# Kernel tuning notes

Measured on AMD Instinct MI355X. Metric: run time of the kernel, lower is better.

Reference implementation:

```python
import jax, jax.numpy as jnp
import numpy as np

B, M, D, P, T = 512, 16, 128, 16, 4096
GAMMA = 1.0  # similarity_size


def setup_inputs() -> dict:
    key = jax.random.key(0)
    k1, k2, k3, k4, k5 = jax.random.split(key, 5)
    phi = jax.random.normal(k1, (B, P), dtype=jnp.float32)
    state = jax.random.normal(k2, (B, D), dtype=jnp.float32)
    trajectories = jax.random.normal(k3, (T, D), dtype=jnp.float32)
    # Stand-in per-model KAARMA state-transition parameters (linear recurrent + input map, tanh)
    A = jax.random.normal(k4, (M, D, D), dtype=jnp.float32) * (1.0 / np.sqrt(D))
    B_in = jax.random.normal(k5, (M, P, D), dtype=jnp.float32) * (1.0 / np.sqrt(P))
    return {"phi": phi, "state": state, "trajectories": trajectories, "A": A, "B_in": B_in}


def reference(phi, state, trajectories, A, B_in):
    # per-model state update: new_state[b,m,:] = tanh(state @ A_m + phi @ B_m)
    new_state = jnp.tanh(
        jnp.einsum("bd,mdh->bmh", state, A) + jnp.einsum("bp,mph->bmh", phi, B_in)
    )  # [B, M, D]
    # RBF similarity vs trajectory set via ||s||^2 + ||t||^2 - 2 s.t (single batched GEMM)
    s_sq = jnp.sum(new_state * new_state, axis=-1, keepdims=True)      # [B, M, 1]
    t_sq = jnp.sum(trajectories * trajectories, axis=-1)               # [T]
    cross = jnp.einsum("bmd,td->bmt", new_state, trajectories)         # [B, M, T]
    sq_dist = jnp.maximum(s_sq + t_sq[None, None, :] - 2.0 * cross, 0.0)
    sim = jnp.exp(-GAMMA * sq_dist)                                    # [B, M, T]
    output = sim.reshape(phi.shape[0], -1)                             # [B, M*T]
    return output, new_state
```

## Files before the change

kernel.cpp:

```cpp
#include <hip/hip_runtime.h>
#include <hip/hip_bf16.h>
#include <cstdint>
#include <cstddef>

#define NB 512
#define NM 16
#define ND 128
#define NP 16
#define NT 4096

typedef __bf16 bf16x8 __attribute__((ext_vector_type(8)));
typedef float f32x4 __attribute__((ext_vector_type(4)));

static_assert(sizeof(bf16x8) == 16, "bf16x8 must be 16B");

__device__ __forceinline__ void gload_lds16(const void* g, void* l) {
  __builtin_amdgcn_global_load_lds(
      (const __attribute__((address_space(1))) unsigned int*)g,
      (__attribute__((address_space(3))) unsigned int*)l, 16, 0, 0);
}

__global__ __launch_bounds__(256) void prep_kernel(
    const float* __restrict__ phi, const float* __restrict__ state,
    const float* __restrict__ traj, const float* __restrict__ A,
    const float* __restrict__ Bin, float* __restrict__ ns_out,
    __bf16* __restrict__ ns_bf, __bf16* __restrict__ tj_bf,
    float* __restrict__ s_sq, float* __restrict__ t_sq) {
  __shared__ alignas(16) float sSt[16 * 128];
  __shared__ alignas(16) float sPhi[16 * 16];
  __shared__ alignas(16) float sRes[16 * 128];
  const int tid = threadIdx.x;
  const int bx = blockIdx.x;

  if (bx < 512) {
    const int m = bx & 15;
    const int b0 = (bx >> 4) * 16;
    const float4* S4 = (const float4*)(state + (size_t)b0 * 128);
    float4* sSt4 = (float4*)sSt;
    sSt4[tid] = S4[tid];
    sSt4[tid + 256] = S4[tid + 256];
    sPhi[tid] = phi[b0 * 16 + tid];
    __syncthreads();

    const int h2 = tid & 63;
    const int rgrp = tid >> 6;
    const float* Ap = A + (size_t)m * 16384 + h2;
    const float* Bp = Bin + (size_t)m * 2048 + h2;

    float acc[2][4];
#pragma unroll
    for (int hi = 0; hi < 2; ++hi)
#pragma unroll
      for (int j = 0; j < 4; ++j) acc[hi][j] = 0.f;

#pragma unroll 4
    for (int c = 0; c < 32; ++c) {
      float a0[4], a1[4];
#pragma unroll
      for (int u = 0; u < 4; ++u) {
        a0[u] = Ap[(size_t)(c * 4 + u) * 128];
        a1[u] = Ap[(size_t)(c * 4 + u) * 128 + 64];
      }
#pragma unroll
      for (int j = 0; j < 4; ++j) {
        const f32x4 sv = *(const f32x4*)&sSt[(rgrp * 4 + j) * 128 + c * 4];
#pragma unroll
        for (int u = 0; u < 4; ++u) {
          acc[0][j] = fmaf(sv[u], a0[u], acc[0][j]);
          acc[1][j] = fmaf(sv[u], a1[u], acc[1][j]);
        }
      }
    }
#pragma unroll
    for (int pc = 0; pc < 4; ++pc) {
      float b0v[4], b1v[4];
#pragma unroll
      for (int u = 0; u < 4; ++u) {
        b0v[u] = Bp[(size_t)(pc * 4 + u) * 128];
        b1v[u] = Bp[(size_t)(pc * 4 + u) * 128 + 64];
      }
#pragma unroll
      for (int j = 0; j < 4; ++j) {
        const f32x4 pv = *(const f32x4*)&sPhi[(rgrp * 4 + j) * 16 + pc * 4];
#pragma unroll
        for (int u = 0; u < 4; ++u) {
          acc[0][j] = fmaf(pv[u], b0v[u], acc[0][j]);
          acc[1][j] = fmaf(pv[u], b1v[u], acc[1][j]);
        }
      }
    }

#pragma unroll
    for (int j = 0; j < 4; ++j) {
      const int row = rgrp * 4 + j;
      const int R = (b0 + row) * 16 + m;
      const float v0 = tanhf(acc[0][j]);
      const float v1 = tanhf(acc[1][j]);
      ns_out[(size_t)R * 128 + h2] = v0;
      ns_out[(size_t)R * 128 + h2 + 64] = v1;
      sRes[row * 128 + h2] = v0;
      sRes[row * 128 + h2 + 64] = v1;
      float s = v0 * v0 + v1 * v1;
#pragma unroll
      for (int o = 32; o > 0; o >>= 1) s += __shfl_xor(s, o);
      if (h2 == 0) s_sq[R] = s;
    }
    __syncthreads();

    {
      const int row = tid >> 4;
      const int kb = tid & 15;
      const f32x4 r0 = *(const f32x4*)&sRes[row * 128 + kb * 8];
      const f32x4 r1 = *(const f32x4*)&sRes[row * 128 + kb * 8 + 4];
      bf16x8 o;
#pragma unroll
      for (int i = 0; i < 4; ++i) {
        o[i] = (__bf16)r0[i];
        o[i + 4] = (__bf16)r1[i];
      }
      const int R = (b0 + row) * 16 + m;
      *(bf16x8*)(ns_bf + (size_t)R * 128 + ((kb ^ m) * 8)) = o;
    }
  } else {
    const int t0 = (bx - 512) * 128;
    const int t = t0 + (tid >> 1);
    const int half = tid & 1;
    float s = 0.f;
#pragma unroll
    for (int q = 0; q < 8; ++q) {
      const int kb = half * 8 + q;
      const f32x4 v0 = *(const f32x4*)&traj[(size_t)t * 128 + kb * 8];
      const f32x4 v1 = *(const f32x4*)&traj[(size_t)t * 128 + kb * 8 + 4];
      s += v0[0] * v0[0] + v0[1] * v0[1] + v0[2] * v0[2] + v0[3] * v0[3];
      s += v1[0] * v1[0] + v1[1] * v1[1] + v1[2] * v1[2] + v1[3] * v1[3];
      bf16x8 o;
#pragma unroll
      for (int i = 0; i < 4; ++i) {
        o[i] = (__bf16)v0[i];
        o[i + 4] = (__bf16)v1[i];
      }
      *(bf16x8*)(tj_bf + (size_t)t * 128 + ((kb ^ (t & 15)) * 8)) = o;
    }
    s += __shfl_xor(s, 1);
    if (half == 0) t_sq[t] = s;
  }
}

__global__ __launch_bounds__(256, 1) void sim_kernel(
    const __bf16* __restrict__ ns_bf, const __bf16* __restrict__ tj_bf,
    const float* __restrict__ s_sq, const float* __restrict__ t_sq,
    float* __restrict__ out) {
  __shared__ alignas(16) __bf16 sNS[128 * 128];
  __shared__ alignas(16) __bf16 sT[2][128 * 128];
  const int tid = threadIdx.x;
  const int lane = tid & 63;
  const int w = tid >> 6;
  const int p = blockIdx.x;
  const int R0 = (p >> 2) * 128;
  const int Cg = (p & 3) * 8;
  const int rbase = (w >> 1) * 64;
  const int cbase = (w & 1) * 64;
  const int l15 = lane & 15;
  const int quad = lane >> 4;

  const char* gNS = (const char*)(ns_bf + (size_t)R0 * 128);
  const char* gT0 = (const char*)(tj_bf + (size_t)(Cg * 128) * 128);
#pragma unroll
  for (int it = 0; it < 8; ++it) {
    const int off = it * 4096 + w * 1024;
    gload_lds16(gNS + off + lane * 16, (char*)sNS + off);
    gload_lds16(gT0 + off + lane * 16, (char*)sT[0] + off);
  }
  __syncthreads();

  bf16x8 af[4][4];
#pragma unroll
  for (int ks = 0; ks < 4; ++ks)
#pragma unroll
    for (int i = 0; i < 4; ++i)
      af[ks][i] = *(const bf16x8*)&sNS[(rbase + i * 16 + l15) * 128 +
                                       (((quad + ks * 4) ^ l15) * 8)];
  float sqr[4];
#pragma unroll
  for (int ri = 0; ri < 4; ++ri)
    sqr[ri] = s_sq[R0 + rbase + ri * 16 + l15];

#pragma unroll
  for (int t = 0; t < 8; ++t) {
    const int cur = t & 1;
    if (t + 1 < 8) {
      const char* gT = (const char*)(tj_bf + (size_t)((Cg + t + 1) * 128) * 128);
#pragma unroll
      for (int it = 0; it < 8; ++it) {
        const int off = it * 4096 + w * 1024;
        gload_lds16(gT + off + lane * 16, (char*)sT[cur ^ 1] + off);
      }
    }

    f32x4 acc[4][4];
#pragma unroll
    for (int i = 0; i < 4; ++i)
#pragma unroll
      for (int j = 0; j < 4; ++j) acc[i][j] = (f32x4){0.f, 0.f, 0.f, 0.f};

    const __bf16* sB = sT[cur];
#pragma unroll
    for (int ks = 0; ks < 4; ++ks) {
      bf16x8 bfr[4];
#pragma unroll
      for (int i = 0; i < 4; ++i)
        bfr[i] = *(const bf16x8*)&sB[(cbase + i * 16 + l15) * 128 +
                                     (((quad + ks * 4) ^ l15) * 8)];
#pragma unroll
      for (int ri = 0; ri < 4; ++ri)
#pragma unroll
        for (int ci = 0; ci < 4; ++ci)
          acc[ri][ci] = __builtin_amdgcn_mfma_f32_16x16x32_bf16(
              bfr[ci], af[ks][ri], acc[ri][ci], 0, 0, 0);
    }

    const int C0 = (Cg + t) * 128;
    f32x4 tq[4];
#pragma unroll
    for (int ci = 0; ci < 4; ++ci)
      tq[ci] = *(const f32x4*)&t_sq[C0 + cbase + ci * 16 + quad * 4];
#pragma unroll
    for (int ri = 0; ri < 4; ++ri) {
      const float sq = sqr[ri];
      float* orow = out + (size_t)(R0 + rbase + ri * 16 + l15) * NT + C0;
#pragma unroll
      for (int ci = 0; ci < 4; ++ci) {
        const int t4 = cbase + ci * 16 + quad * 4;
        f32x4 r;
#pragma unroll
        for (int k = 0; k < 4; ++k) {
          const float d = fmaxf(sq + tq[ci][k] - 2.f * acc[ri][ci][k], 0.f);
          r[k] = __expf(-d);
        }
        *(f32x4*)&orow[t4] = r;
      }
    }
    __syncthreads();
  }
}

extern "C" void kernel_launch(void* const* d_in, const int* in_sizes, int n_in,
                              void* d_out, int out_size, void* d_ws,
                              size_t ws_size, hipStream_t stream) {
  (void)in_sizes; (void)n_in; (void)out_size; (void)ws_size;
  const float* phi   = (const float*)d_in[0];
  const float* state = (const float*)d_in[1];
  const float* traj  = (const float*)d_in[2];
  const float* A     = (const float*)d_in[3];
  const float* Bin   = (const float*)d_in[4];

  float* out = (float*)d_out;
  float* out_ns = out + (size_t)NB * NM * NT;

  char* ws = (char*)d_ws;
  __bf16* ns_bf = (__bf16*)ws;
  __bf16* tj_bf = (__bf16*)(ws + (2u << 20));
  float* s_sq   = (float*)(ws + (3u << 20));
  float* t_sq   = (float*)(ws + (3u << 20) + (32u << 10));

  prep_kernel<<<544, 256, 0, stream>>>(phi, state, traj, A, Bin, out_ns, ns_bf,
                                       tj_bf, s_sq, t_sq);
  sim_kernel<<<256, 256, 0, stream>>>(ns_bf, tj_bf, s_sq, t_sq, out);
}
```

Baseline: 175.0 us.

## Fuse state-update GEMV into similarity kernel and split trajectory prep out

The state update (tanh of state@A + phi@B) now runs inside the similarity kernel. Each block computes 32 rows of new_state for one model and keeps them in LDS as swizzled bf16, so the bf16 state buffer and s_sq no longer round-trip through global memory. Trajectory conversion moves to its own small kernel. The sim tile shrinks to 32 rows by 2048 columns with 512 blocks at two blocks per CU. The cost is that each block pair recomputes the same state GEMV, and the A/B reads are redundant across the two column halves.

Measured after the change: 175.4 us. No clear change (+0.2%).

```diff
diff --git a/kernel.cpp b/kernel.cpp
--- a/kernel.cpp
+++ b/kernel.cpp
@@ -20,224 +20,205 @@
       (__attribute__((address_space(3))) unsigned int*)l, 16, 0, 0);
 }
 
-__global__ __launch_bounds__(256) void prep_kernel(
+__global__ __launch_bounds__(256) void traj_kernel(
+    const float* __restrict__ traj, __bf16* __restrict__ tj_bf,
+    float* __restrict__ t_sq) {
+  const int tid = threadIdx.x;
+  const int t = blockIdx.x * 128 + (tid >> 1);
+  const int half = tid & 1;
+  float s = 0.f;
+#pragma unroll
+  for (int q = 0; q < 8; ++q) {
+    const int kb = half * 8 + q;
+    const f32x4 v0 = *(const f32x4*)&traj[(size_t)t * 128 + kb * 8];
+    const f32x4 v1 = *(const f32x4*)&traj[(size_t)t * 128 + kb * 8 + 4];
+    s += v0[0] * v0[0] + v0[1] * v0[1] + v0[2] * v0[2] + v0[3] * v0[3];
+    s += v1[0] * v1[0] + v1[1] * v1[1] + v1[2] * v1[2] + v1[3] * v1[3];
+    bf16x8 o;
+#pragma unroll
+    for (int i = 0; i < 4; ++i) {
+      o[i] = (__bf16)v0[i];
+      o[i + 4] = (__bf16)v1[i];
+    }
+    *(bf16x8*)(tj_bf + (size_t)t * 128 + ((kb ^ (t & 15)) * 8)) = o;
+  }
+  s += __shfl_xor(s, 1);
+  if (half == 0) t_sq[t] = s;
+}
+
+__global__ __launch_bounds__(256, 2) void fused_kernel(
     const float* __restrict__ phi, const float* __restrict__ state,
-    const float* __restrict__ traj, const float* __restrict__ A,
-    const float* __restrict__ Bin, float* __restrict__ ns_out,
-    __bf16* __restrict__ ns_bf, __bf16* __restrict__ tj_bf,
-    float* __restrict__ s_sq, float* __restrict__ t_sq) {
-  __shared__ alignas(16) float sSt[16 * 128];
-  __shared__ alignas(16) float sPhi[16 * 16];
-  __shared__ alignas(16) float sRes[16 * 128];
-  const int tid = threadIdx.x;
-  const int bx = blockIdx.x;
-
-  if (bx < 512) {
-    const int m = bx & 15;
-    const int b0 = (bx >> 4) * 16;
-    const float4* S4 = (const float4*)(state + (size_t)b0 * 128);
-    float4* sSt4 = (float4*)sSt;
-    sSt4[tid] = S4[tid];
-    sSt4[tid + 256] = S4[tid + 256];
-    sPhi[tid] = phi[b0 * 16 + tid];
-    __syncthreads();
-
-    const int h2 = tid & 63;
-    const int rgrp = tid >> 6;
-    const float* Ap = A + (size_t)m * 16384 + h2;
-    const float* Bp = Bin + (size_t)m * 2048 + h2;
-
-    float acc[2][4];
-#pragma unroll
-    for (int hi = 0; hi < 2; ++hi)
-#pragma unroll
-      for (int j = 0; j < 4; ++j) acc[hi][j] = 0.f;
-
-#pragma unroll 4
-    for (int c = 0; c < 32; ++c) {
-      float a0[4], a1[4];
-#pragma unroll
-      for (int u = 0; u < 4; ++u) {
-        a0[u] = Ap[(size_t)(c * 4 + u) * 128];
-        a1[u] = Ap[(size_t)(c * 4 + u) * 128 + 64];
-      }
-#pragma unroll
-      for (int j = 0; j < 4; ++j) {
-        const f32x4 sv = *(const f32x4*)&sSt[(rgrp * 4 + j) * 128 + c * 4];
-#pragma unroll
-        for (int u = 0; u < 4; ++u) {
-          acc[0][j] = fmaf(sv[u], a0[u], acc[0][j]);
-          acc[1][j] = fmaf(sv[u], a1[u], acc[1][j]);
-        }
-      }
-    }
-#pragma unroll
-    for (int pc = 0; pc < 4; ++pc) {
-      float b0v[4], b1v[4];
-#pragma unroll
-      for (int u = 0; u < 4; ++u) {
-        b0v[u] = Bp[(size_t)(pc * 4 + u) * 128];
-        b1v[u] = Bp[(size_t)(pc * 4 + u) * 128 + 64];
-      }
-#pragma unroll
-      for (int j = 0; j < 4; ++j) {
-        const f32x4 pv = *(const f32x4*)&sPhi[(rgrp * 4 + j) * 16 + pc * 4];
-#pragma unroll
-        for (int u = 0; u < 4; ++u) {
-          acc[0][j] = fmaf(pv[u], b0v[u], acc[0][j]);
-          acc[1][j] = fmaf(pv[u], b1v[u], acc[1][j]);
-        }
-      }
-    }
-
-#pragma unroll
-    for (int j = 0; j < 4; ++j) {
-      const int row = rgrp * 4 + j;
-      const int R = (b0 + row) * 16 + m;
-      const float v0 = tanhf(acc[0][j]);
-      const float v1 = tanhf(acc[1][j]);
-      ns_out[(size_t)R * 128 + h2] = v0;
-      ns_out[(size_t)R * 128 + h2 + 64] = v1;
-      sRes[row * 128 + h2] = v0;
-      sRes[row * 128 + h2 + 64] = v1;
-      float s = v0 * v0 + v1 * v1;
-#pragma unroll
-      for (int o = 32; o > 0; o >>= 1) s += __shfl_xor(s, o);
-      if (h2 == 0) s_sq[R] = s;
-    }
-    __syncthreads();
-
-    {
-      const int row = tid >> 4;
-      const int kb = tid & 15;
-      const f32x4 r0 = *(const f32x4*)&sRes[row * 128 + kb * 8];
-      const f32x4 r1 = *(const f32x4*)&sRes[row * 128 + kb * 8 + 4];
-      bf16x8 o;
-#pragma unroll
-      for (int i = 0; i < 4; ++i) {
-        o[i] = (__bf16)r0[i];
-        o[i + 4] = (__bf16)r1[i];
-      }
-      const int R = (b0 + row) * 16 + m;
-      *(bf16x8*)(ns_bf + (size_t)R * 128 + ((kb ^ m) * 8)) = o;
-    }
-  } else {
-    const int t0 = (bx - 512) * 128;
-    const int t = t0 + (tid >> 1);
-    const int half = tid & 1;
-    float s = 0.f;
-#pragma unroll
-    for (int q = 0; q < 8; ++q) {
-      const int kb = half * 8 + q;
-      const f32x4 v0 = *(const f32x4*)&traj[(size_t)t * 128 + kb * 8];
-      const f32x4 v1 = *(const f32x4*)&traj[(size_t)t * 128 + kb * 8 + 4];
-      s += v0[0] * v0[0] + v0[1] * v0[1] + v0[2] * v0[2] + v0[3] * v0[3];
-      s += v1[0] * v1[0] + v1[1] * v1[1] + v1[2] * v1[2] + v1[3] * v1[3];
-      bf16x8 o;
-#pragma unroll
-      for (int i = 0; i < 4; ++i) {
-        o[i] = (__bf16)v0[i];
-        o[i + 4] = (__bf16)v1[i];
-      }
-      *(bf16x8*)(tj_bf + (size_t)t * 128 + ((kb ^ (t & 15)) * 8)) = o;
-    }
-    s += __shfl_xor(s, 1);
-    if (half == 0) t_sq[t] = s;
-  }
-}
-
-__global__ __launch_bounds__(256, 1) void sim_kernel(
-    const __bf16* __restrict__ ns_bf, const __bf16* __restrict__ tj_bf,
-    const float* __restrict__ s_sq, const float* __restrict__ t_sq,
-    float* __restrict__ out) {
-  __shared__ alignas(16) __bf16 sNS[128 * 128];
-  __shared__ alignas(16) __bf16 sT[2][128 * 128];
+    const float* __restrict__ A, const float* __restrict__ Bin,
+    const __bf16* __restrict__ tj_bf, const float* __restrict__ t_sq,
+    float* __restrict__ ns_out, float* __restrict__ out) {
+  __shared__ alignas(16) char smem[75904];
+  char* sT0 = smem;
+  char* sT1 = smem + 32768;
+  float* sSt = (float*)(smem + 32768);
+  __bf16* sNS = (__bf16*)(smem + 65536);
+  float* sSq = (float*)(smem + 73728);
+  float* sPhi = (float*)(smem + 73856);
+
   const int tid = threadIdx.x;
   const int lane = tid & 63;
   const int w = tid >> 6;
   const int p = blockIdx.x;
-  const int R0 = (p >> 2) * 128;
-  const int Cg = (p & 3) * 8;
-  const int rbase = (w >> 1) * 64;
-  const int cbase = (w & 1) * 64;
+  const int pan = p >> 1;
+  const int ch = p & 1;
+  const int m = pan & 15;
+  const int b0 = (pan >> 4) * 32;
+  const int tt0 = ch * 16;
+
+  {
+    const float4* S4 = (const float4*)(state + (size_t)b0 * 128);
+    float4* sSt4 = (float4*)sSt;
+#pragma unroll
+    for (int q = 0; q < 4; ++q) sSt4[tid + q * 256] = S4[tid + q * 256];
+    sPhi[tid] = phi[b0 * 16 + tid];
+    sPhi[tid + 256] = phi[b0 * 16 + tid + 256];
+  }
+  __syncthreads();
+
+  {
+    const char* gT = (const char*)tj_bf + (size_t)tt0 * 32768;
+#pragma unroll
+    for (int it = 0; it < 8; ++it) {
+      const int off = it * 4096 + w * 1024;
+      gload_lds16(gT + off + lane * 16, sT0 + off);
+    }
+  }
+
+  const int h2 = lane;
+  const float* Ap = A + (size_t)m * 16384 + h2;
+  const float* Bp = Bin + (size_t)m * 2048 + h2;
+  float acc0[8], acc1[8];
+#pragma unroll
+  for (int j = 0; j < 8; ++j) { acc0[j] = 0.f; acc1[j] = 0.f; }
+
+#pragma unroll 4
+  for (int c = 0; c < 32; ++c) {
+    float a0[4], a1[4];
+#pragma unroll
+    for (int u = 0; u < 4; ++u) {
+      a0[u] = Ap[(size_t)(c * 4 + u) * 128];
+      a1[u] = Ap[(size_t)(c * 4 + u) * 128 + 64];
+    }
+#pragma unroll
+    for (int j = 0; j < 8; ++j) {
+      const f32x4 sv = *(const f32x4*)&sSt[(w * 8 + j) * 128 + c * 4];
+#pragma unroll
+      for (int u = 0; u < 4; ++u) {
+        acc0[j] = fmaf(sv[u], a0[u], acc0[j]);
+        acc1[j] = fmaf(sv[u], a1[u], acc1[j]);
+      }
+    }
+  }
+#pragma unroll
+  for (int pc = 0; pc < 4; ++pc) {
+    float b0v[4], b1v[4];
+#pragma unroll
+    for (int u = 0; u < 4; ++u) {
+      b0v[u] = Bp[(size_t)(pc * 4 + u) * 128];
+      b1v[u] = Bp[(size_t)(pc * 4 + u) * 128 + 64];
+    }
+#pragma unroll
+    for (int j = 0; j < 8; ++j) {
+      const f32x4 pv = *(const f32x4*)&sPhi[(w * 8 + j) * 16 + pc * 4];
+#pragma unroll
+      for (int u = 0; u < 4; ++u) {
+        acc0[j] = fmaf(pv[u], b0v[u], acc0[j]);
+        acc1[j] = fmaf(pv[u], b1v[u], acc1[j]);
+      }
+    }
+  }
+
+#pragma unroll
+  for (int j = 0; j < 8; ++j) {
+    const int r = w * 8 + j;
+    const int R = (b0 + r) * 16 + m;
+    const float v0 = tanhf(acc0[j]);
+    const float v1 = tanhf(acc1[j]);
+    if (ch == 0) {
+      ns_out[(size_t)R * 128 + h2] = v0;
+      ns_out[(size_t)R * 128 + h2 + 64] = v1;
+    }
+    const int kb0 = h2 >> 3;
+    sNS[r * 128 + ((kb0 ^ (r & 15)) << 3) + (h2 & 7)] = (__bf16)v0;
+    sNS[r * 128 + (((kb0 + 8) ^ (r & 15)) << 3) + (h2 & 7)] = (__bf16)v1;
+    float s = v0 * v0 + v1 * v1;
+#pragma unroll
+    for (int o = 32; o > 0; o >>= 1) s += __shfl_xor(s, o);
+    if (lane == 0) sSq[r] = s;
+  }
+  __syncthreads();
+
   const int l15 = lane & 15;
   const int quad = lane >> 4;
-
-  const char* gNS = (const char*)(ns_bf + (size_t)R0 * 128);
-  const char* gT0 = (const char*)(tj_bf + (size_t)(Cg * 128) * 128);
-#pragma unroll
-  for (int it = 0; it < 8; ++it) {
-    const int off = it * 4096 + w * 1024;
-    gload_lds16(gNS + off + lane * 16, (char*)sNS + off);
-    gload_lds16(gT0 + off + lane * 16, (char*)sT[0] + off);
-  }
-  __syncthreads();
-
-  bf16x8 af[4][4];
+  bf16x8 af[4][2];
 #pragma unroll
   for (int ks = 0; ks < 4; ++ks)
 #pragma unroll
-    for (int i = 0; i < 4; ++i)
-      af[ks][i] = *(const bf16x8*)&sNS[(rbase + i * 16 + l15) * 128 +
-                                       (((quad + ks * 4) ^ l15) * 8)];
-  float sqr[4];
-#pragma unroll
-  for (int ri = 0; ri < 4; ++ri)
-    sqr[ri] = s_sq[R0 + rbase + ri * 16 + l15];
-
-#pragma unroll
-  for (int t = 0; t < 8; ++t) {
-    const int cur = t & 1;
-    if (t + 1 < 8) {
-      const char* gT = (const char*)(tj_bf + (size_t)((Cg + t + 1) * 128) * 128);
+    for (int ri = 0; ri < 2; ++ri)
+      af[ks][ri] = *(const bf16x8*)&sNS[(ri * 16 + l15) * 128 +
+                                        (((quad + ks * 4) ^ l15) * 8)];
+  float sqr[2];
+#pragma unroll
+  for (int ri = 0; ri < 2; ++ri) sqr[ri] = sSq[ri * 16 + l15];
+
+#pragma unroll 2
+  for (int t = 0; t < 16; ++t) {
+    const char* curbuf = (t & 1) ? sT1 : sT0;
+    if (t + 1 < 16) {
+      char* nxt = (t & 1) ? sT0 : sT1;
+      const char* gT = (const char*)tj_bf + (size_t)(tt0 + t + 1) * 32768;
 #pragma unroll
       for (int it = 0; it < 8; ++it) {
         const int off = it * 4096 + w * 1024;
-        gload_lds16(gT + off + lane * 16, (char*)sT[cur ^ 1] + off);
-      }
-    }
-
-    f32x4 acc[4][4];
-#pragma unroll
-    for (int i = 0; i < 4; ++i)
-#pragma unroll
-      for (int j = 0; j < 4; ++j) acc[i][j] = (f32x4){0.f, 0.f, 0.f, 0.f};
-
-    const __bf16* sB = sT[cur];
+        gload_lds16(gT + off + lane * 16, nxt + off);
+      }
+    }
+
+    const __bf16* sB = (const __bf16*)curbuf;
+    f32x4 acc[2][2];
+#pragma unroll
+    for (int i = 0; i < 2; ++i)
+#pragma unroll
+      for (int j = 0; j < 2; ++j) acc[i][j] = (f32x4){0.f, 0.f, 0.f, 0.f};
+
 #pragma unroll
     for (int ks = 0; ks < 4; ++ks) {
-      bf16x8 bfr[4];
-#pragma unroll
-      for (int i = 0; i < 4; ++i)
-        bfr[i] = *(const bf16x8*)&sB[(cbase + i * 16 + l15) * 128 +
-                                     (((quad + ks * 4) ^ l15) * 8)];
-#pragma unroll
-      for (int ri = 0; ri < 4; ++ri)
-#pragma unroll
-        for (int ci = 0; ci < 4; ++ci)
+      bf16x8 bfr[2];
+#pragma unroll
+      for (int ci = 0; ci < 2; ++ci)
+        bfr[ci] = *(const bf16x8*)&sB[(w * 32 + ci * 16 + l15) * 128 +
+                                      (((quad + ks * 4) ^ l15) * 8)];
+#pragma unroll
+      for (int ri = 0; ri < 2; ++ri)
+#pragma unroll
+        for (int ci = 0; ci < 2; ++ci)
           acc[ri][ci] = __builtin_amdgcn_mfma_f32_16x16x32_bf16(
               bfr[ci], af[ks][ri], acc[ri][ci], 0, 0, 0);
     }
 
-    const int C0 = (Cg + t) * 128;
-    f32x4 tq[4];
-#pragma unroll
-    for (int ci = 0; ci < 4; ++ci)
-      tq[ci] = *(const f32x4*)&t_sq[C0 + cbase + ci * 16 + quad * 4];
-#pragma unroll
-    for (int ri = 0; ri < 4; ++ri) {
+    const int C0 = (tt0 + t) * 128;
+    f32x4 tq[2];
+#pragma unroll
+    for (int ci = 0; ci < 2; ++ci)
+      tq[ci] = *(const f32x4*)&t_sq[C0 + w * 32 + ci * 16 + quad * 4];
+#pragma unroll
+    for (int ri = 0; ri < 2; ++ri) {
+      const int r = ri * 16 + l15;
       const float sq = sqr[ri];
-      float* orow = out + (size_t)(R0 + rbase + ri * 16 + l15) * NT + C0;
-#pragma unroll
-      for (int ci = 0; ci < 4; ++ci) {
-        const int t4 = cbase + ci * 16 + quad * 4;
-        f32x4 r;
+      float* orow = out + (size_t)((b0 + r) * 16 + m) * NT + C0;
+#pragma unroll
+      for (int ci = 0; ci < 2; ++ci) {
+        f32x4 rr;
 #pragma unroll
         for (int k = 0; k < 4; ++k) {
           const float d = fmaxf(sq + tq[ci][k] - 2.f * acc[ri][ci][k], 0.f);
-          r[k] = __expf(-d);
+          rr[k] = __expf(-d);
         }
-        *(f32x4*)&orow[t4] = r;
+        *(f32x4*)&orow[w * 32 + ci * 16 + quad * 4] = rr;
       }
     }
     __syncthreads();
@@ -258,12 +239,10 @@
   float* out_ns = out + (size_t)NB * NM * NT;
 
   char* ws = (char*)d_ws;
-  __bf16* ns_bf = (__bf16*)ws;
-  __bf16* tj_bf = (__bf16*)(ws + (2u << 20));
-  float* s_sq   = (float*)(ws + (3u << 20));
-  float* t_sq   = (float*)(ws + (3u << 20) + (32u << 10));
-
-  prep_kernel<<<544, 256, 0, stream>>>(phi, state, traj, A, Bin, out_ns, ns_bf,
-                                       tj_bf, s_sq, t_sq);
-  sim_kernel<<<256, 256, 0, stream>>>(ns_bf, tj_bf, s_sq, t_sq, out);
-}
+  __bf16* tj_bf = (__bf16*)ws;
+  float* t_sq   = (float*)(ws + (1u << 20));
+
+  traj_kernel<<<32, 256, 0, stream>>>(traj, tj_bf, t_sq);
+  fused_kernel<<<512, 256, 0, stream>>>(phi, state, A, Bin, tj_bf, t_sq,
+                                        out_ns, out);
+}
```

## Halve sim kernel LDS footprint and double grid for two blocks per CU

Applied to the files above, without the earlier changes.

The state tile and the trajectory double buffer now share two 32KB LDS buffers. The state fragments are moved to registers first, and then that buffer is reused for trajectory prefetch. Launch bounds allow two blocks per CU, and the grid doubles to 512 blocks, each covering 4 trajectory tiles instead of 8. This is meant to raise occupancy and hide latency in the output-store-bound epilogue, at the cost of a register cap and more redundant state loads.

New measurement: 170.1 us. 2.8% less time.

```diff
diff --git a/kernel.cpp b/kernel.cpp
--- a/kernel.cpp
+++ b/kernel.cpp
@@ -146,30 +146,29 @@
   }
 }
 
-__global__ __launch_bounds__(256, 1) void sim_kernel(
+__global__ __launch_bounds__(256, 2) void sim_kernel(
     const __bf16* __restrict__ ns_bf, const __bf16* __restrict__ tj_bf,
     const float* __restrict__ s_sq, const float* __restrict__ t_sq,
     float* __restrict__ out) {
-  __shared__ alignas(16) __bf16 sNS[128 * 128];
-  __shared__ alignas(16) __bf16 sT[2][128 * 128];
+  __shared__ alignas(16) __bf16 sBuf[2][128 * 128];
   const int tid = threadIdx.x;
   const int lane = tid & 63;
   const int w = tid >> 6;
   const int p = blockIdx.x;
-  const int R0 = (p >> 2) * 128;
-  const int Cg = (p & 3) * 8;
+  const int R0 = (p >> 3) * 128;
+  const int ct0 = (p & 7) * 4;
   const int rbase = (w >> 1) * 64;
   const int cbase = (w & 1) * 64;
   const int l15 = lane & 15;
   const int quad = lane >> 4;
 
   const char* gNS = (const char*)(ns_bf + (size_t)R0 * 128);
-  const char* gT0 = (const char*)(tj_bf + (size_t)(Cg * 128) * 128);
+  const char* gT0 = (const char*)(tj_bf + (size_t)ct0 * 16384);
 #pragma unroll
   for (int it = 0; it < 8; ++it) {
     const int off = it * 4096 + w * 1024;
-    gload_lds16(gNS + off + lane * 16, (char*)sNS + off);
-    gload_lds16(gT0 + off + lane * 16, (char*)sT[0] + off);
+    gload_lds16(gNS + off + lane * 16, (char*)sBuf[0] + off);
+    gload_lds16(gT0 + off + lane * 16, (char*)sBuf[1] + off);
   }
   __syncthreads();
 
@@ -177,40 +176,40 @@
 #pragma unroll
   for (int ks = 0; ks < 4; ++ks)
 #pragma unroll
-    for (int i = 0; i < 4; ++i)
-      af[ks][i] = *(const bf16x8*)&sNS[(rbase + i * 16 + l15) * 128 +
-                                       (((quad + ks * 4) ^ l15) * 8)];
+    for (int ri = 0; ri < 4; ++ri)
+      af[ks][ri] = *(const bf16x8*)&sBuf[0][(rbase + ri * 16 + l15) * 128 +
+                                           (((quad + ks * 4) ^ l15) * 8)];
   float sqr[4];
 #pragma unroll
-  for (int ri = 0; ri < 4; ++ri)
-    sqr[ri] = s_sq[R0 + rbase + ri * 16 + l15];
-
-#pragma unroll
-  for (int t = 0; t < 8; ++t) {
-    const int cur = t & 1;
-    if (t + 1 < 8) {
-      const char* gT = (const char*)(tj_bf + (size_t)((Cg + t + 1) * 128) * 128);
+  for (int ri = 0; ri < 4; ++ri) sqr[ri] = s_sq[R0 + rbase + ri * 16 + l15];
+  __syncthreads();
+
+#pragma unroll
+  for (int t = 0; t < 4; ++t) {
+    if (t < 3) {
+      char* nxt = (char*)sBuf[t & 1];
+      const char* gT = (const char*)(tj_bf + (size_t)(ct0 + t + 1) * 16384);
 #pragma unroll
       for (int it = 0; it < 8; ++it) {
         const int off = it * 4096 + w * 1024;
-        gload_lds16(gT + off + lane * 16, (char*)sT[cur ^ 1] + off);
-      }
-    }
-
+        gload_lds16(gT + off + lane * 16, nxt + off);
+      }
+    }
+
+    const __bf16* sB = sBuf[(t & 1) ^ 1];
     f32x4 acc[4][4];
 #pragma unroll
     for (int i = 0; i < 4; ++i)
 #pragma unroll
       for (int j = 0; j < 4; ++j) acc[i][j] = (f32x4){0.f, 0.f, 0.f, 0.f};
 
-    const __bf16* sB = sT[cur];
 #pragma unroll
     for (int ks = 0; ks < 4; ++ks) {
       bf16x8 bfr[4];
 #pragma unroll
-      for (int i = 0; i < 4; ++i)
-        bfr[i] = *(const bf16x8*)&sB[(cbase + i * 16 + l15) * 128 +
-                                     (((quad + ks * 4) ^ l15) * 8)];
+      for (int ci = 0; ci < 4; ++ci)
+        bfr[ci] = *(const bf16x8*)&sB[(cbase + ci * 16 + l15) * 128 +
+                                      (((quad + ks * 4) ^ l15) * 8)];
 #pragma unroll
       for (int ri = 0; ri < 4; ++ri)
 #pragma unroll
@@ -219,7 +218,7 @@
               bfr[ci], af[ks][ri], acc[ri][ci], 0, 0, 0);
     }
 
-    const int C0 = (Cg + t) * 128;
+    const int C0 = (ct0 + t) * 128;
     f32x4 tq[4];
 #pragma unroll
     for (int ci = 0; ci < 4; ++ci)
@@ -265,5 +264,5 @@
 
   prep_kernel<<<544, 256, 0, stream>>>(phi, state, traj, A, Bin, out_ns, ns_bf,
                                        tj_bf, s_sq, t_sq);
-  sim_kernel<<<256, 256, 0, stream>>>(ns_bf, tj_bf, s_sq, t_sq, out);
-}
+  sim_kernel<<<512, 256, 0, stream>>>(ns_bf, tj_bf, s_sq, t_sq, out);
+}
```
